# Kernel tuning notes

Hardware: AMD Instinct MI355X
Metric: run time of the kernel (lower is better)

## Reference

```python
import jax, jax.numpy as jnp
import numpy as np

EPS = 1e-8
R_CUT = 4.8
NEW_NB = 20  # hardcoded neighbor truncation in the original forward
B = 32768
NB = 64


def setup_inputs() -> dict:
    key = jax.random.key(0)
    ks = jax.random.split(key, 9)
    # dr: random directions with radii in [1.5, 4.5] so R > ecode (tanh^2 <= 1);
    # this avoids NaN from negative base with fractional exponent (same hazard exists in torch).
    raw = jax.random.normal(ks[0], (B, NB, 3), dtype=jnp.float32)
    direction = raw / jnp.linalg.norm(raw, axis=-1, keepdims=True)
    radius = 1.5 + 3.0 * jax.random.uniform(ks[1], (B, NB, 1), dtype=jnp.float32)
    dr = direction * radius
    orientation = jax.random.normal(ks[2], (B, 3, 3), dtype=jnp.float32)
    n_orientation = jax.random.normal(ks[3], (B, NB, 3, 3), dtype=jnp.float32)

    def lin(k, fan_in, fan_out):
        s = 1.0 / np.sqrt(fan_in)
        kw, kb = jax.random.split(k)
        W = jax.random.uniform(kw, (fan_in, fan_out), jnp.float32, -s, s)
        b = jax.random.uniform(kb, (fan_out,), jnp.float32, -s, s)
        return W, b

    W0, b0 = lin(ks[4], 15, 64)
    W1, b1 = lin(ks[5], 64, 64)
    W2, b2 = lin(ks[6], 64, 1)
    f1 = jax.random.uniform(ks[7], (3, 1), dtype=jnp.float32)
    f2 = jax.random.uniform(ks[8], (3, 1), dtype=jnp.float32)
    return dict(dr=dr, orientation=orientation, n_orientation=n_orientation,
                W0=W0, b0=b0, W1=W1, b1=b1, W2=W2, b2=b2, f1=f1, f2=f2)


def _prior_net(x, W0, b0, W1, b1, W2, b2):
    # Linear-tanh-Linear-tanh-Linear (dropout inactive at eval)
    h = jnp.tanh(x @ W0 + b0)
    h = jnp.tanh(h @ W1 + b1)
    return h @ W2 + b2


def _energy(new_dr_norm, orientation, new_R, new_n_or, fcR, W0, b0, W1, b1, W2, b2, f1, f2):
    b, n = new_dr_norm.shape[:2]
    dr_o = jnp.einsum('bnk,bkh->bnh', new_dr_norm, orientation)            # [B,20,3]
    dr_no = jnp.einsum('bnk,bnkh->bnh', new_dr_norm, new_n_or)             # [B,20,3]
    o_no = jnp.einsum('bhl,bnhm->bnlm', orientation, new_n_or).reshape(b, n, 9)
    feat = jnp.concatenate([dr_o, dr_no, o_no], axis=-1)                   # [B,20,15]
    enc = jnp.tanh(_prior_net(feat, W0, b0, W1, b1, W2, b2))               # [B,20,1]
    ecode = (enc ** 2 + EPS)[..., None, None]                              # [B,20,1,1,1]
    prior = new_R[..., None, None] - ecode                                 # [B,20,1,1,1]
    prior = (f1 ** 2 + EPS) * prior                                        # [B,20,1,3,1]
    prior = prior ** (-(f2 ** 2 + EPS))                                    # power-law
    prior = prior.sum(axis=3).reshape(b, n, 1)                             # [B,20,1]
    energy = prior.sum(axis=1, keepdims=True) * fcR                        # [B,20,1]
    return energy


def _forward(dr, orientation, n_orientation, W0, b0, W1, b1, W2, b2, f1, f2):
    b = dr.shape[0]
    dr = dr + EPS
    R = jnp.linalg.norm(dr, axis=-1, keepdims=True)                        # [B,Nb,1]
    dr_norm = dr / R
    idx = jnp.argsort(R, axis=1)[:, :NEW_NB, :]                            # [B,20,1]
    new_R = jnp.take_along_axis(R, idx, axis=1)                            # [B,20,1]
    new_dr_norm = jnp.take_along_axis(dr_norm, jnp.broadcast_to(idx, (b, NEW_NB, 3)), axis=1)
    new_n_or = jnp.take_along_axis(n_orientation, jnp.broadcast_to(idx[..., None], (b, NEW_NB, 3, 3)), axis=1)
    fcR = jnp.where(new_R > R_CUT, 0.0, 0.5 * jnp.cos(jnp.pi * new_R / R_CUT) + 0.5)

    def esum(ndn, orient):
        e = _energy(ndn, orient, new_R, new_n_or, fcR, W0, b0, W1, b1, W2, b2, f1, f2)
        return e.sum(), e

    # mirrors torch.autograd.grad(energy.sum(), (new_dr_norm, orientation), create_graph=True)
    (_, energy), (g_dr, g_or) = jax.value_and_grad(esum, argnums=(0, 1), has_aux=True)(new_dr_norm, orientation)
    force = g_dr.sum(axis=1)                                               # [B,3]
    torque = (jnp.cross(g_or[:, :, 0], orientation[:, :, 0])
              + jnp.cross(g_or[:, :, 1], orientation[:, :, 1])
              + jnp.cross(g_or[:, :, 2], orientation[:, :, 2]))            # [B,3]
    return force, torque, energy


def reference(dr, orientation, n_orientation, W0, b0, W1, b1, W2, b2, f1, f2):
    return _forward(dr, orientation, n_orientation, W0, b0, W1, b1, W2, b2, f1, f2)
```

## Files before the change

kernel.cpp:

```cpp
#include <hip/hip_runtime.h>

#define EPSF 1e-8f
#define RCUT 4.8f
#define NB 64
#define NSEL 20

__device__ __forceinline__ float fast_tanh(float x) {
    float e = __expf(2.0f * x);
    return 1.0f - __fdividef(2.0f, e + 1.0f);
}

extern "C" __global__ void __launch_bounds__(256)
sel_kernel(const float* __restrict__ dr, const float* __restrict__ W0,
           float* __restrict__ ws_R, float* __restrict__ ws_fc,
           float* __restrict__ ws_F, int* __restrict__ ws_idx,
           float* __restrict__ ws_ndn, float* __restrict__ ws_W0T)
{
    __shared__ float R_s[256];
    const int t = threadIdx.x;
    const int g = t >> 6;
    const int j = t & 63;
    const int b = blockIdx.x * 4 + g;

    const float* p = dr + ((size_t)b * NB + j) * 3;
    float x = p[0] + EPSF, y = p[1] + EPSF, z = p[2] + EPSF;
    float R = sqrtf(x * x + y * y + z * z);
    R_s[t] = R;
    __syncthreads();

    int rank = 0;
    const float* grp = R_s + g * 64;
    #pragma unroll 8
    for (int k = 0; k < 64; ++k) {
        float Rk = grp[k];
        rank += (Rk < R || (Rk == R && k < j)) ? 1 : 0;
    }

    float fc = 0.0f;
    if (rank < NSEL) {
        fc = (R > RCUT) ? 0.0f
                        : (0.5f * __cosf(3.14159265358979323846f * R / RCUT) + 0.5f);
        size_t o = (size_t)b * NSEL + rank;
        ws_R[o]  = R;
        ws_fc[o] = fc;
        ws_idx[o] = j;
        float inv = 1.0f / R;
        ws_ndn[o * 3 + 0] = x * inv;
        ws_ndn[o * 3 + 1] = y * inv;
        ws_ndn[o * 3 + 2] = z * inv;
    }

    float F = fc;
    for (int off = 32; off > 0; off >>= 1) F += __shfl_xor(F, off, 64);
    if (j == 0) ws_F[b] = F;

    if (blockIdx.x == 0) {
        for (int i = t; i < 15 * 64; i += 256) {
            int k = i >> 6, jj = i & 63;
            ws_W0T[jj * 15 + k] = W0[i];
        }
    }
}

extern "C" __global__ void __launch_bounds__(320, 4)
energy_kernel(const float* __restrict__ orientation, const float* __restrict__ n_or,
              const float* __restrict__ W0T, const float* __restrict__ b0,
              const float* __restrict__ W1, const float* __restrict__ b1,
              const float* __restrict__ W2, const float* __restrict__ b2v,
              const float* __restrict__ f1, const float* __restrict__ f2,
              const float* __restrict__ ws_R, const float* __restrict__ ws_fc,
              const float* __restrict__ ws_F, const int* __restrict__ ws_idx,
              const float* __restrict__ ws_ndn,
              float* __restrict__ out_force, float* __restrict__ out_torque,
              float* __restrict__ out_energy)
{
    __shared__ float p_s[320];
    __shared__ float red[320][12];
    __shared__ float G[16][12];

    const int t = threadIdx.x;
    const int bl = t / 20;
    const int n  = t % 20;
    const int b  = blockIdx.x * 16 + bl;
    const size_t o = (size_t)b * NSEL + n;

    float feat[15];
    {
        const float nd0 = ws_ndn[o * 3 + 0];
        const float nd1 = ws_ndn[o * 3 + 1];
        const float nd2 = ws_ndn[o * 3 + 2];
        const int  idx = ws_idx[o];
        float O[9], Nr[9];
        const float* Op = orientation + (size_t)b * 9;
        #pragma unroll
        for (int i = 0; i < 9; ++i) O[i] = Op[i];
        const float* Np = n_or + ((size_t)b * NB + idx) * 9;
        #pragma unroll
        for (int i = 0; i < 9; ++i) Nr[i] = Np[i];

        #pragma unroll
        for (int h = 0; h < 3; ++h)
            feat[h] = nd0 * O[h] + nd1 * O[3 + h] + nd2 * O[6 + h];
        #pragma unroll
        for (int h = 0; h < 3; ++h)
            feat[3 + h] = nd0 * Nr[h] + nd1 * Nr[3 + h] + nd2 * Nr[6 + h];
        #pragma unroll
        for (int l = 0; l < 3; ++l)
            #pragma unroll
            for (int m = 0; m < 3; ++m)
                feat[6 + l * 3 + m] = O[l] * Nr[m] + O[3 + l] * Nr[3 + m] + O[6 + l] * Nr[6 + m];
    }

    float acc[64];
    #pragma unroll
    for (int i = 0; i < 64; ++i) acc[i] = b1[i];

    for (int j = 0; j < 64; j += 2) {
        const float* w0a = W0T + j * 15;
        const float* w0b = w0a + 15;
        float za = b0[j], zb = b0[j + 1];
        #pragma unroll
        for (int k = 0; k < 15; ++k) {
            za = fmaf(feat[k], w0a[k], za);
            zb = fmaf(feat[k], w0b[k], zb);
        }
        float ha = fast_tanh(za), hb = fast_tanh(zb);
        const float* w1a = W1 + j * 64;
        const float* w1b = w1a + 64;
        #pragma unroll
        for (int i = 0; i < 64; ++i)
            acc[i] = fmaf(hb, w1b[i], fmaf(ha, w1a[i], acc[i]));
    }

    float z30 = b2v[0], z31 = 0.f, z32 = 0.f, z33 = 0.f;
    #pragma unroll
    for (int i = 0; i < 64; i += 4) {
        acc[i]     = fast_tanh(acc[i]);
        acc[i + 1] = fast_tanh(acc[i + 1]);
        acc[i + 2] = fast_tanh(acc[i + 2]);
        acc[i + 3] = fast_tanh(acc[i + 3]);
        z30 = fmaf(acc[i],     W2[i],     z30);
        z31 = fmaf(acc[i + 1], W2[i + 1], z31);
        z32 = fmaf(acc[i + 2], W2[i + 2], z32);
        z33 = fmaf(acc[i + 3], W2[i + 3], z33);
    }
    const float enc = fast_tanh((z30 + z31) + (z32 + z33));
    float x;
    {
        const volatile float* Rv = ws_R + o;
        x = Rv[0] - (enc * enc + EPSF);
    }

    const float lx = __logf(x);
    float psum = 0.f, csum = 0.f;
    #pragma unroll
    for (int q = 0; q < 3; ++q) {
        float aq = f1[q] * f1[q] + EPSF;
        float cq = f2[q] * f2[q] + EPSF;
        float tq = __expf(-cq * (__logf(aq) + lx));
        psum += tq;
        csum = fmaf(cq, tq, csum);
    }
    const float dpdx = -__fdividef(csum, x);

    p_s[t] = psum;
    __syncthreads();
    {
        float S = 0.f;
        for (int m = 0; m < 20; ++m) S += p_s[bl * 20 + m];
        const volatile float* fcv = ws_fc + o;
        out_energy[o] = S * fcv[0];
    }

    float dz3;
    {
        const volatile float* Fv = ws_F + b;
        dz3 = Fv[0] * dpdx * (-2.f * enc) * (1.f - enc * enc);
    }
    #pragma unroll
    for (int i = 0; i < 64; ++i) {
        float h2 = acc[i];
        acc[i] = dz3 * W2[i] * (1.f - h2 * h2);
    }

    float dfeat[15];
    #pragma unroll
    for (int k = 0; k < 15; ++k) dfeat[k] = 0.f;

    for (int j = 0; j < 64; j += 2) {
        const float* w1a = W1 + j * 64;
        const float* w1b = w1a + 64;
        float sa0 = 0.f, sa1 = 0.f, sb0 = 0.f, sb1 = 0.f;
        #pragma unroll
        for (int i = 0; i < 64; i += 2) {
            sa0 = fmaf(acc[i],     w1a[i],     sa0);
            sa1 = fmaf(acc[i + 1], w1a[i + 1], sa1);
            sb0 = fmaf(acc[i],     w1b[i],     sb0);
            sb1 = fmaf(acc[i + 1], w1b[i + 1], sb1);
        }
        float dha = sa0 + sa1, dhb = sb0 + sb1;
        const float* w0a = W0T + j * 15;
        const float* w0b = w0a + 15;
        float za = b0[j], zb = b0[j + 1];
        #pragma unroll
        for (int k = 0; k < 15; ++k) {
            za = fmaf(feat[k], w0a[k], za);
            zb = fmaf(feat[k], w0b[k], zb);
        }
        float ha = fast_tanh(za), hb = fast_tanh(zb);
        float dza = dha * (1.f - ha * ha);
        float dzb = dhb * (1.f - hb * hb);
        #pragma unroll
        for (int k = 0; k < 15; ++k)
            dfeat[k] = fmaf(dzb, w0b[k], fmaf(dza, w0a[k], dfeat[k]));
    }

    float O[9], Nr[9], nd0, nd1, nd2;
    {
        const volatile int* iv = ws_idx + o;
        const int idx = iv[0];
        const volatile float* Ov = orientation + (size_t)b * 9;
        const volatile float* Nv = n_or + ((size_t)b * NB + idx) * 9;
        #pragma unroll
        for (int i = 0; i < 9; ++i) O[i] = Ov[i];
        #pragma unroll
        for (int i = 0; i < 9; ++i) Nr[i] = Nv[i];
        const volatile float* nv = ws_ndn + o * 3;
        nd0 = nv[0]; nd1 = nv[1]; nd2 = nv[2];
    }

    float gdr[3];
    #pragma unroll
    for (int k = 0; k < 3; ++k)
        gdr[k] = dfeat[0] * O[k * 3] + dfeat[1] * O[k * 3 + 1] + dfeat[2] * O[k * 3 + 2]
               + dfeat[3] * Nr[k * 3] + dfeat[4] * Nr[k * 3 + 1] + dfeat[5] * Nr[k * 3 + 2];

    float ndv[3] = {nd0, nd1, nd2};
    float gO[9];
    #pragma unroll
    for (int k = 0; k < 3; ++k)
        #pragma unroll
        for (int h = 0; h < 3; ++h)
            gO[k * 3 + h] = dfeat[h] * ndv[k];
    #pragma unroll
    for (int h = 0; h < 3; ++h)
        #pragma unroll
        for (int l = 0; l < 3; ++l) {
            float s = 0.f;
            #pragma unroll
            for (int m = 0; m < 3; ++m) s = fmaf(dfeat[6 + l * 3 + m], Nr[h * 3 + m], s);
            gO[h * 3 + l] += s;
        }

    #pragma unroll
    for (int q = 0; q < 3; ++q) red[t][q] = gdr[q];
    #pragma unroll
    for (int q = 0; q < 9; ++q) red[t][3 + q] = gO[q];
    __syncthreads();

    for (int i = t; i < 16 * 12; i += 320) {
        int bb = i / 12, q = i % 12;
        float s = 0.f;
        for (int m = 0; m < 20; ++m) s += red[bb * 20 + m][q];
        G[bb][q] = s;
    }
    __syncthreads();

    if (t < 16) {
        const int gb = blockIdx.x * 16 + t;
        out_force[gb * 3 + 0] = G[t][0];
        out_force[gb * 3 + 1] = G[t][1];
        out_force[gb * 3 + 2] = G[t][2];
        const float* Og = orientation + (size_t)gb * 9;
        float t0 = 0.f, t1 = 0.f, t2 = 0.f;
        #pragma unroll
        for (int jj = 0; jj < 3; ++jj) {
            float u0 = G[t][3 + 0 * 3 + jj], u1 = G[t][3 + 1 * 3 + jj], u2 = G[t][3 + 2 * 3 + jj];
            float v0 = Og[0 * 3 + jj], v1 = Og[1 * 3 + jj], v2 = Og[2 * 3 + jj];
            t0 += u1 * v2 - u2 * v1;
            t1 += u2 * v0 - u0 * v2;
            t2 += u0 * v1 - u1 * v0;
        }
        out_torque[gb * 3 + 0] = t0;
        out_torque[gb * 3 + 1] = t1;
        out_torque[gb * 3 + 2] = t2;
    }
}

extern "C" void kernel_launch(void* const* d_in, const int* in_sizes, int n_in,
                              void* d_out, int out_size, void* d_ws, size_t ws_size,
                              hipStream_t stream) {
    const float* dr            = (const float*)d_in[0];
    const float* orientation   = (const float*)d_in[1];
    const float* n_orientation = (const float*)d_in[2];
    const float* W0 = (const float*)d_in[3];
    const float* b0 = (const float*)d_in[4];
    const float* W1 = (const float*)d_in[5];
    const float* b1 = (const float*)d_in[6];
    const float* W2 = (const float*)d_in[7];
    const float* b2 = (const float*)d_in[8];
    const float* f1 = (const float*)d_in[9];
    const float* f2 = (const float*)d_in[10];

    const int B = in_sizes[0] / (NB * 3);

    float* out = (float*)d_out;
    float* out_force  = out;
    float* out_torque = out + (size_t)3 * B;
    float* out_energy = out + (size_t)6 * B;

    float* ws_R   = (float*)d_ws;
    float* ws_fc  = ws_R  + (size_t)B * NSEL;
    float* ws_F   = ws_fc + (size_t)B * NSEL;
    int*   ws_idx = (int*)(ws_F + B);
    float* ws_ndn = (float*)(ws_idx + (size_t)B * NSEL);
    float* ws_W0T = ws_ndn + (size_t)B * NSEL * 3;

    sel_kernel<<<B / 4, 256, 0, stream>>>(dr, W0, ws_R, ws_fc, ws_F, ws_idx, ws_ndn, ws_W0T);
    energy_kernel<<<B / 16, 320, 0, stream>>>(orientation, n_orientation,
                                              ws_W0T, b0, W1, b1, W2, b2, f1, f2,
                                              ws_R, ws_fc, ws_F, ws_idx, ws_ndn,
                                              out_force, out_torque, out_energy);
}
```

Before: 500.9 us.

## Pre-gather selected neighbor orientations in selection kernel and cache in LDS

The selection kernel now reads every neighbor's 3x3 orientation and writes the 20 selected ones contiguously into a workspace buffer, so the energy kernel does coalesced loads instead of indexed gathers. This path is used only when the workspace is large enough. The energy kernel also keeps each thread's neighbor matrix in shared memory so the backward pass does not re-gather it from global memory, and the transposed W0 rows are padded to a stride of 16. In exchange, the selection kernel now reads all 64 neighbor matrices instead of 20, the workspace writes grow, and the extra shared memory may lower occupancy.

```diff
diff --git a/kernel.cpp b/kernel.cpp
--- a/kernel.cpp
+++ b/kernel.cpp
@@ -11,10 +11,12 @@
 }
 
 extern "C" __global__ void __launch_bounds__(256)
-sel_kernel(const float* __restrict__ dr, const float* __restrict__ W0,
+sel_kernel(const float* __restrict__ dr, const float* __restrict__ n_or,
+           const float* __restrict__ W0,
            float* __restrict__ ws_R, float* __restrict__ ws_fc,
            float* __restrict__ ws_F, int* __restrict__ ws_idx,
-           float* __restrict__ ws_ndn, float* __restrict__ ws_W0T)
+           float* __restrict__ ws_ndn, float* __restrict__ ws_W0T,
+           float* __restrict__ ws_nor)
 {
     __shared__ float R_s[256];
     const int t = threadIdx.x;
@@ -50,6 +52,18 @@
         ws_ndn[o * 3 + 2] = z * inv;
     }
 
+    if (ws_nor) {
+        const float* np = n_or + ((size_t)b * NB + j) * 9;
+        float r[9];
+        #pragma unroll
+        for (int q = 0; q < 9; ++q) r[q] = np[q];
+        if (rank < NSEL) {
+            float* dst = ws_nor + ((size_t)b * NSEL + rank) * 9;
+            #pragma unroll
+            for (int q = 0; q < 9; ++q) dst[q] = r[q];
+        }
+    }
+
     float F = fc;
     for (int off = 32; off > 0; off >>= 1) F += __shfl_xor(F, off, 64);
     if (j == 0) ws_F[b] = F;
@@ -57,23 +71,25 @@
     if (blockIdx.x == 0) {
         for (int i = t; i < 15 * 64; i += 256) {
             int k = i >> 6, jj = i & 63;
-            ws_W0T[jj * 15 + k] = W0[i];
+            ws_W0T[jj * 16 + k] = W0[i];
         }
     }
 }
 
-extern "C" __global__ void __launch_bounds__(320, 4)
-energy_kernel(const float* __restrict__ orientation, const float* __restrict__ n_or,
+template<bool PRE>
+__global__ void __launch_bounds__(320, 4)
+energy_kernel_t(const float* __restrict__ orientation, const float* __restrict__ n_or,
               const float* __restrict__ W0T, const float* __restrict__ b0,
               const float* __restrict__ W1, const float* __restrict__ b1,
               const float* __restrict__ W2, const float* __restrict__ b2v,
               const float* __restrict__ f1, const float* __restrict__ f2,
               const float* __restrict__ ws_R, const float* __restrict__ ws_fc,
               const float* __restrict__ ws_F, const int* __restrict__ ws_idx,
-              const float* __restrict__ ws_ndn,
+              const float* __restrict__ ws_ndn, const float* __restrict__ ws_nor,
               float* __restrict__ out_force, float* __restrict__ out_torque,
               float* __restrict__ out_energy)
 {
+    __shared__ float sNr[320 * 9];
     __shared__ float p_s[320];
     __shared__ float red[320][12];
     __shared__ float G[16][12];
@@ -89,14 +105,22 @@
         const float nd0 = ws_ndn[o * 3 + 0];
         const float nd1 = ws_ndn[o * 3 + 1];
         const float nd2 = ws_ndn[o * 3 + 2];
-        const int  idx = ws_idx[o];
         float O[9], Nr[9];
         const float* Op = orientation + (size_t)b * 9;
         #pragma unroll
         for (int i = 0; i < 9; ++i) O[i] = Op[i];
-        const float* Np = n_or + ((size_t)b * NB + idx) * 9;
-        #pragma unroll
-        for (int i = 0; i < 9; ++i) Nr[i] = Np[i];
+        if (PRE) {
+            const float* Np = ws_nor + o * 9;
+            #pragma unroll
+            for (int i = 0; i < 9; ++i) Nr[i] = Np[i];
+        } else {
+            const int idx = ws_idx[o];
+            const float* Np = n_or + ((size_t)b * NB + idx) * 9;
+            #pragma unroll
+            for (int i = 0; i < 9; ++i) Nr[i] = Np[i];
+        }
+        #pragma unroll
+        for (int q = 0; q < 9; ++q) sNr[t * 9 + q] = Nr[q];
 
         #pragma unroll
         for (int h = 0; h < 3; ++h)
@@ -116,8 +140,8 @@
     for (int i = 0; i < 64; ++i) acc[i] = b1[i];
 
     for (int j = 0; j < 64; j += 2) {
-        const float* w0a = W0T + j * 15;
-        const float* w0b = w0a + 15;
+        const float* w0a = W0T + j * 16;
+        const float* w0b = w0a + 16;
         float za = b0[j], zb = b0[j + 1];
         #pragma unroll
         for (int k = 0; k < 15; ++k) {
@@ -199,8 +223,8 @@
             sb1 = fmaf(acc[i + 1], w1b[i + 1], sb1);
         }
         float dha = sa0 + sa1, dhb = sb0 + sb1;
-        const float* w0a = W0T + j * 15;
-        const float* w0b = w0a + 15;
+        const float* w0a = W0T + j * 16;
+        const float* w0b = w0a + 16;
         float za = b0[j], zb = b0[j + 1];
         #pragma unroll
         for (int k = 0; k < 15; ++k) {
@@ -217,14 +241,12 @@
 
     float O[9], Nr[9], nd0, nd1, nd2;
     {
-        const volatile int* iv = ws_idx + o;
-        const int idx = iv[0];
         const volatile float* Ov = orientation + (size_t)b * 9;
-        const volatile float* Nv = n_or + ((size_t)b * NB + idx) * 9;
         #pragma unroll
         for (int i = 0; i < 9; ++i) O[i] = Ov[i];
-        #pragma unroll
-        for (int i = 0; i < 9; ++i) Nr[i] = Nv[i];
+        volatile float* sv = sNr + t * 9;
+        #pragma unroll
+        for (int i = 0; i < 9; ++i) Nr[i] = sv[i];
         const volatile float* nv = ws_ndn + o * 3;
         nd0 = nv[0]; nd1 = nv[1]; nd2 = nv[2];
     }
@@ -310,15 +332,29 @@
     float* out_energy = out + (size_t)6 * B;
 
     float* ws_R   = (float*)d_ws;
-    float* ws_fc  = ws_R  + (size_t)B * NSEL;
-    float* ws_F   = ws_fc + (size_t)B * NSEL;
+    float* ws_fc  = ws_R   + (size_t)B * NSEL;
+    float* ws_F   = ws_fc  + (size_t)B * NSEL;
     int*   ws_idx = (int*)(ws_F + B);
     float* ws_ndn = (float*)(ws_idx + (size_t)B * NSEL);
     float* ws_W0T = ws_ndn + (size_t)B * NSEL * 3;
-
-    sel_kernel<<<B / 4, 256, 0, stream>>>(dr, W0, ws_R, ws_fc, ws_F, ws_idx, ws_ndn, ws_W0T);
-    energy_kernel<<<B / 16, 320, 0, stream>>>(orientation, n_orientation,
-                                              ws_W0T, b0, W1, b1, W2, b2, f1, f2,
-                                              ws_R, ws_fc, ws_F, ws_idx, ws_ndn,
-                                              out_force, out_torque, out_energy);
+    float* ws_nor = ws_W0T + 1024;
+
+    const size_t needed_full = sizeof(float) *
+        ((size_t)B * (NSEL * (1 + 1 + 1 + 3 + 9)) + (size_t)B + 1024);
+    const bool pre = ws_size >= needed_full;
+
+    sel_kernel<<<B / 4, 256, 0, stream>>>(dr, n_orientation, W0,
+                                          ws_R, ws_fc, ws_F, ws_idx, ws_ndn, ws_W0T,
+                                          pre ? ws_nor : nullptr);
+    if (pre) {
+        energy_kernel_t<true><<<B / 16, 320, 0, stream>>>(orientation, n_orientation,
+            ws_W0T, b0, W1, b1, W2, b2, f1, f2,
+            ws_R, ws_fc, ws_F, ws_idx, ws_ndn, ws_nor,
+            out_force, out_torque, out_energy);
+    } else {
+        energy_kernel_t<false><<<B / 16, 320, 0, stream>>>(orientation, n_orientation,
+            ws_W0T, b0, W1, b1, W2, b2, f1, f2,
+            ws_R, ws_fc, ws_F, ws_idx, ws_ndn, ws_nor,
+            out_force, out_torque, out_energy);
+    }
 }
```

After: 502.0 us. About the same (+0.2%).
